# Kernel tuning notes

Hardware: AMD Instinct MI355X
Metric: run time of the kernel (lower is better)

## Reference

```python
import jax, jax.numpy as jnp
import numpy as np

OUT_H, OUT_W = 512, 512
BATCH, CHANNELS = 64, 3


def setup_inputs() -> dict:
    key = jax.random.key(0)
    k1, k2 = jax.random.split(key)
    U = jax.random.normal(k1, (BATCH, OUT_H, OUT_W, CHANNELS), dtype=jnp.float32)
    theta = jax.random.normal(k2, (BATCH, 1), dtype=jnp.float32)
    return {"U": U, "theta": theta}


def reference(U, theta):
    B = U.shape[0]
    H, W = OUT_H, OUT_W
    # normalized sampling grid [H*W, 3] with homogeneous coordinate
    gx, gy = jnp.meshgrid(jnp.linspace(-1.0, 1.0, W), jnp.linspace(-1.0, 1.0, H))
    grid = jnp.stack([gx, gy, jnp.ones_like(gx)], axis=-1).reshape(H * W, 3)
    # rotation-only affine matrix [B, 2, 3]
    cos_t, sin_t, z = jnp.cos(theta), jnp.sin(theta), jnp.zeros_like(theta)
    rot = jnp.concatenate([cos_t, -sin_t, z, sin_t, cos_t, z], axis=1).reshape(B, 2, 3)
    # transformed source coords [B, H*W, 2]
    T_g = jnp.einsum('bij,nj->bni', rot, grid)
    x = (T_g[..., 0] + 1.0) * (W - 1) / 2.0
    y = (T_g[..., 1] + 1.0) * (H - 1) / 2.0
    x0f = jnp.floor(x).astype(jnp.int32)
    y0f = jnp.floor(y).astype(jnp.int32)
    x0 = jnp.clip(x0f, 0, W - 1)
    x1 = jnp.clip(x0f + 1, 0, W - 1)
    y0 = jnp.clip(y0f, 0, H - 1)
    y1 = jnp.clip(y0f + 1, 0, H - 1)
    # 4-corner gathers, batched: [B, H*W, C]
    gather = jax.vmap(lambda u, yy, xx: u[yy, xx])
    Ia = gather(U, y0, x0)
    Ib = gather(U, y1, x0)
    Ic = gather(U, y0, x1)
    Id = gather(U, y1, x1)
    x0_f, x1_f = x0.astype(jnp.float32), x1.astype(jnp.float32)
    y0_f, y1_f = y0.astype(jnp.float32), y1.astype(jnp.float32)
    wa = (x1_f - x) * (y1_f - y)
    wb = (x1_f - x) * (y - y0_f)
    wc = (x - x0_f) * (y1_f - y)
    wd = (x - x0_f) * (y - y0_f)
    out = (wa[..., None] * Ia + wb[..., None] * Ib
           + wc[..., None] * Ic + wd[..., None] * Id)
    return out.reshape(B, H, W, -1)
```

## Files before the change

### kernel.cpp

```cpp
#include <hip/hip_runtime.h>
#include <hip/hip_fp16.h>

#define OUT_H 512
#define OUT_W 512
#define BATCH 64
#define CHANS 3

#define WROWS 48
#define WPX   48
#define PITCH 49
#define PLANE (WROWS * PITCH)
#define IDXMAX (PLANE - PITCH - 2)

__global__ __launch_bounds__(256) void st_bilinear_kernel(
    const float* __restrict__ U,
    const float* __restrict__ theta,
    float* __restrict__ out)
{
    __shared__ __align__(16) unsigned int smA[PLANE];
    __shared__ __align__(16) unsigned int smB[PLANE];

    int blk  = blockIdx.x;
    int lblk = (blk & 7) * 2048 + (blk >> 3);

    int b  = lblk >> 8;
    int t  = lblk & 255;
    int i0 = (t >> 4) << 5;
    int j0 = (t & 15) << 5;

    int tid = threadIdx.x;

    float tt = theta[__builtin_amdgcn_readfirstlane(b)];
    float s, c;
    __sincosf(tt, &s, &c);

    const float scale = 2.0f / 511.0f;
    float gx0 = (float)j0 * scale - 1.0f;
    float gy0 = (float)i0 * scale - 1.0f;
    float xb0 = (c * gx0 - s * gy0 + 1.0f) * 255.5f;
    float yb0 = (s * gx0 + c * gy0 + 1.0f) * 255.5f;

    float xmin = xb0 + fminf(0.0f, 31.0f * c) + fminf(0.0f, -31.0f * s);
    float ymin = yb0 + fminf(0.0f, 31.0f * s) + fminf(0.0f,  31.0f * c);

    int bx0 = min(max((int)floorf(xmin), 0), OUT_W - 1);
    int by0 = min(max((int)floorf(ymin), 0), OUT_H - 1);
    int bx_load = min(bx0, OUT_W - WPX);
    int by_load = min(by0, OUT_H - WROWS);

    const float* Ub = U + (size_t)b * (OUT_H * OUT_W * CHANS);
    const float* gb = Ub + ((size_t)by_load * OUT_W + bx_load) * CHANS;

    float2 lc01[9];
    float  lc2[9];
#pragma unroll
    for (int k = 0; k < 9; ++k) {
        unsigned q = (unsigned)tid + 256u * k;
        unsigned r  = q / 48u;
        unsigned lx = q - r * 48u;
        const float* p = gb + (size_t)r * (OUT_W * CHANS) + lx * 3u;
        lc01[k] = *(const float2*)p;
        lc2[k]  = p[2];
    }
#pragma unroll
    for (int k = 0; k < 9; ++k) {
        unsigned q = (unsigned)tid + 256u * k;
        unsigned r  = q / 48u;
        unsigned lx = q - r * 48u;
        unsigned slot = r * PITCH + lx;
        __half2 h01 = __floats2half2_rn(lc01[k].x, lc01[k].y);
        __half2 h2  = __floats2half2_rn(lc2[k], 0.0f);
        smA[slot] = *(const unsigned int*)&h01;
        smB[slot] = *(const unsigned int*)&h2;
    }
    __syncthreads();

    int il = tid >> 3;
    int jb = (tid & 7) << 2;
    float xr = xb0 + c * (float)jb - s * (float)il;
    float yr = yb0 + s * (float)jb + c * (float)il;
    int Koff = by_load * PITCH + bx_load;

    float o[12];
#pragma unroll
    for (int p = 0; p < 4; ++p) {
        float x = fmaf(c, (float)p, xr);
        float y = fmaf(s, (float)p, yr);

        int ix = __float2int_rd(x);
        int iy = __float2int_rd(y);
        float fx = x - (float)ix;
        float fy = y - (float)iy;

        int idx = iy * PITCH + ix - Koff;
        idx = min(max(idx, 0), IDXMAX);

        unsigned iA0 = smA[idx],         iA1 = smA[idx + 1];
        unsigned iA2 = smA[idx + PITCH], iA3 = smA[idx + PITCH + 1];
        unsigned iB0 = smB[idx],         iB1 = smB[idx + 1];
        unsigned iB2 = smB[idx + PITCH], iB3 = smB[idx + PITCH + 1];

        __half2 fx2 = __float2half2_rn(fx);
        __half2 fy2 = __float2half2_rn(fy);
        __half2 a01 = *(const __half2*)&iA0, c01 = *(const __half2*)&iA1;
        __half2 b01 = *(const __half2*)&iA2, d01 = *(const __half2*)&iA3;
        __half2 a2  = *(const __half2*)&iB0, c2  = *(const __half2*)&iB1;
        __half2 b2  = *(const __half2*)&iB2, d2  = *(const __half2*)&iB3;

        __half2 t01 = __hfma2(fx2, __hsub2(c01, a01), a01);
        __half2 t2  = __hfma2(fx2, __hsub2(c2,  a2),  a2);
        __half2 u01 = __hfma2(fx2, __hsub2(d01, b01), b01);
        __half2 u2  = __hfma2(fx2, __hsub2(d2,  b2),  b2);
        __half2 r01 = __hfma2(fy2, __hsub2(u01, t01), t01);
        __half2 r2  = __hfma2(fy2, __hsub2(u2,  t2),  t2);

        bool valid = (x >= 0.0f) && (x < 511.0f) && (y >= 0.0f) && (y < 511.0f);
        o[p * 3 + 0] = valid ? __low2float(r01)  : 0.0f;
        o[p * 3 + 1] = valid ? __high2float(r01) : 0.0f;
        o[p * 3 + 2] = valid ? __low2float(r2)   : 0.0f;
    }

    float* po = out + (((size_t)b * OUT_H + (i0 + il)) * OUT_W + (j0 + jb)) * CHANS;
    ((float4*)po)[0] = make_float4(o[0], o[1], o[2],  o[3]);
    ((float4*)po)[1] = make_float4(o[4], o[5], o[6],  o[7]);
    ((float4*)po)[2] = make_float4(o[8], o[9], o[10], o[11]);
}

extern "C" void kernel_launch(void* const* d_in, const int* in_sizes, int n_in,
                              void* d_out, int out_size, void* d_ws, size_t ws_size,
                              hipStream_t stream) {
    const float* U     = (const float*)d_in[0];
    const float* theta = (const float*)d_in[1];
    float* out = (float*)d_out;

    int blocks = BATCH * (OUT_H / 32) * (OUT_W / 32);
    st_bilinear_kernel<<<blocks, 256, 0, stream>>>(U, theta, out);
}
```

Before: 100.9 us.

## Interleave LDS planes per row, use float4 staging loads, skip clamps for interior tiles

```diff
diff --git a/kernel.cpp b/kernel.cpp
--- a/kernel.cpp
+++ b/kernel.cpp
@@ -8,17 +8,16 @@
 
 #define WROWS 48
 #define WPX   48
-#define PITCH 49
-#define PLANE (WROWS * PITCH)
-#define IDXMAX (PLANE - PITCH - 2)
+#define RSTRIDE 98
+#define LSZ 4704
+#define IDXMAX (LSZ - 149)
 
 __global__ __launch_bounds__(256) void st_bilinear_kernel(
     const float* __restrict__ U,
     const float* __restrict__ theta,
     float* __restrict__ out)
 {
-    __shared__ __align__(16) unsigned int smA[PLANE];
-    __shared__ __align__(16) unsigned int smB[PLANE];
+    __shared__ __align__(16) unsigned int smf[LSZ];
 
     int blk  = blockIdx.x;
     int lblk = (blk & 7) * 2048 + (blk >> 3);
@@ -42,36 +41,53 @@
 
     float xmin = xb0 + fminf(0.0f, 31.0f * c) + fminf(0.0f, -31.0f * s);
     float ymin = yb0 + fminf(0.0f, 31.0f * s) + fminf(0.0f,  31.0f * c);
+    float xmax = xb0 + fmaxf(0.0f, 31.0f * c) + fmaxf(0.0f, -31.0f * s);
+    float ymax = yb0 + fmaxf(0.0f, 31.0f * s) + fmaxf(0.0f,  31.0f * c);
 
     int bx0 = min(max((int)floorf(xmin), 0), OUT_W - 1);
     int by0 = min(max((int)floorf(ymin), 0), OUT_H - 1);
     int bx_load = min(bx0, OUT_W - WPX);
     int by_load = min(by0, OUT_H - WROWS);
 
+    bool interior = (xmin >= 0.0f) & (xmax < 510.0f) &
+                    (ymin >= 0.0f) & (ymax < 510.0f);
+
     const float* Ub = U + (size_t)b * (OUT_H * OUT_W * CHANS);
     const float* gb = Ub + ((size_t)by_load * OUT_W + bx_load) * CHANS;
 
-    float2 lc01[9];
-    float  lc2[9];
+    float4 va[9];
+    bool origin = (b == 0) & (bx_load == 0) & (by_load == 0);
+    if (!origin) {
 #pragma unroll
-    for (int k = 0; k < 9; ++k) {
-        unsigned q = (unsigned)tid + 256u * k;
-        unsigned r  = q / 48u;
-        unsigned lx = q - r * 48u;
-        const float* p = gb + (size_t)r * (OUT_W * CHANS) + lx * 3u;
-        lc01[k] = *(const float2*)p;
-        lc2[k]  = p[2];
+        for (int k = 0; k < 9; ++k) {
+            unsigned q = (unsigned)tid + 256u * k;
+            unsigned r  = q / 48u;
+            unsigned lx = q - r * 48u;
+            va[k] = *(const float4*)(gb + (size_t)r * (OUT_W * CHANS) + lx * 3u - 1);
+        }
+    } else {
+#pragma unroll
+        for (int k = 0; k < 9; ++k) {
+            unsigned q = (unsigned)tid + 256u * k;
+            unsigned r  = q / 48u;
+            unsigned lx = q - r * 48u;
+            const float* p = gb + (size_t)r * (OUT_W * CHANS) + lx * 3u;
+            float2 ab = *(const float2*)p;
+            float  cc = p[2];
+            va[k] = make_float4(0.0f, ab.x, ab.y, cc);
+        }
     }
 #pragma unroll
     for (int k = 0; k < 9; ++k) {
         unsigned q = (unsigned)tid + 256u * k;
         unsigned r  = q / 48u;
         unsigned lx = q - r * 48u;
-        unsigned slot = r * PITCH + lx;
-        __half2 h01 = __floats2half2_rn(lc01[k].x, lc01[k].y);
-        __half2 h2  = __floats2half2_rn(lc2[k], 0.0f);
-        smA[slot] = *(const unsigned int*)&h01;
-        smB[slot] = *(const unsigned int*)&h2;
+        unsigned slot = RSTRIDE * r + lx;
+        float4 v = va[k];
+        __half2 hA = __floats2half2_rn(v.y, v.z);
+        __half2 hB = __floats2half2_rn(v.w, 0.0f);
+        smf[slot]      = *(const unsigned int*)&hA;
+        smf[slot + 49] = *(const unsigned int*)&hB;
     }
     __syncthreads();
 
@@ -79,32 +95,32 @@
     int jb = (tid & 7) << 2;
     float xr = xb0 + c * (float)jb - s * (float)il;
     float yr = yb0 + s * (float)jb + c * (float)il;
-    int Koff = by_load * PITCH + bx_load;
+    int Koff = by_load * RSTRIDE + bx_load;
 
     float o[12];
 #pragma unroll
     for (int p = 0; p < 4; ++p) {
         float x = fmaf(c, (float)p, xr);
         float y = fmaf(s, (float)p, yr);
-
         int ix = __float2int_rd(x);
         int iy = __float2int_rd(y);
         float fx = x - (float)ix;
         float fy = y - (float)iy;
 
-        int idx = iy * PITCH + ix - Koff;
-        idx = min(max(idx, 0), IDXMAX);
+        int idx = iy * RSTRIDE + ix - Koff;
+        if (!interior) idx = min(max(idx, 0), IDXMAX);
 
-        unsigned iA0 = smA[idx],         iA1 = smA[idx + 1];
-        unsigned iA2 = smA[idx + PITCH], iA3 = smA[idx + PITCH + 1];
-        unsigned iB0 = smB[idx],         iB1 = smB[idx + 1];
-        unsigned iB2 = smB[idx + PITCH], iB3 = smB[idx + PITCH + 1];
+        const unsigned int* lp = smf + idx;
+        unsigned iA0 = lp[0],   iA1 = lp[1];
+        unsigned iB0 = lp[49],  iB1 = lp[50];
+        unsigned iA2 = lp[98],  iA3 = lp[99];
+        unsigned iB2 = lp[147], iB3 = lp[148];
 
         __half2 fx2 = __float2half2_rn(fx);
         __half2 fy2 = __float2half2_rn(fy);
         __half2 a01 = *(const __half2*)&iA0, c01 = *(const __half2*)&iA1;
+        __half2 a2  = *(const __half2*)&iB0, c2  = *(const __half2*)&iB1;
         __half2 b01 = *(const __half2*)&iA2, d01 = *(const __half2*)&iA3;
-        __half2 a2  = *(const __half2*)&iB0, c2  = *(const __half2*)&iB1;
         __half2 b2  = *(const __half2*)&iB2, d2  = *(const __half2*)&iB3;
 
         __half2 t01 = __hfma2(fx2, __hsub2(c01, a01), a01);
@@ -114,10 +130,18 @@
         __half2 r01 = __hfma2(fy2, __hsub2(u01, t01), t01);
         __half2 r2  = __hfma2(fy2, __hsub2(u2,  t2),  t2);
 
-        bool valid = (x >= 0.0f) && (x < 511.0f) && (y >= 0.0f) && (y < 511.0f);
-        o[p * 3 + 0] = valid ? __low2float(r01)  : 0.0f;
-        o[p * 3 + 1] = valid ? __high2float(r01) : 0.0f;
-        o[p * 3 + 2] = valid ? __low2float(r2)   : 0.0f;
+        float v0 = __low2float(r01);
+        float v1 = __high2float(r01);
+        float v2 = __low2float(r2);
+        if (!interior) {
+            bool valid = ((unsigned)ix < 511u) & ((unsigned)iy < 511u);
+            v0 = valid ? v0 : 0.0f;
+            v1 = valid ? v1 : 0.0f;
+            v2 = valid ? v2 : 0.0f;
+        }
+        o[p * 3 + 0] = v0;
+        o[p * 3 + 1] = v1;
+        o[p * 3 + 2] = v2;
     }
 
     float* po = out + (((size_t)b * OUT_H + (i0 + il)) * OUT_W + (j0 + jb)) * CHANS;
```

Measured after the change: 103.0 us. 2.2% more time.
